# Kernel tuning notes

Hardware: AMD Instinct MI355X
Metric: run time of the kernel (lower is better)

The kernel has to match this reference:

```python
import jax, jax.numpy as jnp
import numpy as np

NULL_IDX = 0  # word_to_idx['<NULL>']
N, T, D, WV, H, V = 128, 65, 512, 128, 128, 10000


def setup_inputs() -> dict:
    key = jax.random.key(0)
    ks = jax.random.split(key, 12)
    scale = 0.02
    return {
        "features": jax.random.normal(ks[0], (N, D), dtype=jnp.float32),
        "captions": jax.random.randint(ks[1], (N, T), 0, V, dtype=jnp.int32),
        # TemporalAffine(input_dim, hidden_dim)
        "W_proj": jax.random.normal(ks[2], (D, H), dtype=jnp.float32) * scale,
        "b_proj": jnp.zeros((H,), dtype=jnp.float32),
        # nn.Embedding(vocab_size, wordvec_dim)
        "embed": jax.random.normal(ks[3], (V, WV), dtype=jnp.float32) * scale,
        # nn.RNN(wordvec_dim, hidden_dim, num_layers=1) weights
        "W_ih": jax.random.normal(ks[4], (H, WV), dtype=jnp.float32) * scale,
        "W_hh": jax.random.normal(ks[5], (H, H), dtype=jnp.float32) * scale,
        "b_ih": jnp.zeros((H,), dtype=jnp.float32),
        "b_hh": jnp.zeros((H,), dtype=jnp.float32),
        # TemporalAffine(hidden_dim, vocab_size)
        "W_vocab": jax.random.normal(ks[6], (H, V), dtype=jnp.float32) * scale,
        "b_vocab": jnp.zeros((V,), dtype=jnp.float32),
    }


def reference(features, captions, W_proj, b_proj, embed, W_ih, W_hh, b_ih, b_hh, W_vocab, b_vocab):
    captions_in = captions[:, :-1]   # (N, T-1)
    captions_out = captions[:, 1:]   # (N, T-1)
    mask = (captions_out != NULL_IDX).astype(jnp.float32)

    # initial hidden state: affine projection of image features (no tanh)
    h0 = features @ W_proj + b_proj                      # (N, H)

    # word embeddings, time-major for scan
    x = embed[captions_in]                               # (N, T-1, WV)
    x_tm = jnp.swapaxes(x, 0, 1)                          # (T-1, N, WV)

    def step(h_prev, x_t):
        # vanilla RNN cell: tanh(x W_ih^T + b_ih + h W_hh^T + b_hh)
        h_new = jnp.tanh(x_t @ W_ih.T + b_ih + h_prev @ W_hh.T + b_hh)
        return h_new, h_new

    _, hs = jax.lax.scan(step, h0, x_tm)                  # (T-1, N, H)
    h = jnp.swapaxes(hs, 0, 1)                            # (N, T-1, H)

    # temporal affine to vocab scores
    scores = h @ W_vocab + b_vocab                        # (N, T-1, V)

    # temporal softmax loss, masked, averaged over batch size N
    logp = jax.nn.log_softmax(scores, axis=-1)
    nll = -jnp.take_along_axis(logp, captions_out[..., None], axis=-1)[..., 0]
    loss = jnp.sum(nll * mask) / captions.shape[0]
    return loss
```

## Files before the change

kernel.cpp:

```cpp
#include <hip/hip_runtime.h>
#include <hip/hip_bf16.h>
#include <math.h>

typedef __attribute__((ext_vector_type(8))) short short8;
typedef __attribute__((ext_vector_type(4))) float f32x4;
typedef __attribute__((ext_vector_type(4))) unsigned int u32x4;

#define NB   128
#define TT   64
#define DD   512
#define HH   128
#define WVD  128
#define VV   10000
#define VP   10048
#define NROW (NB*TT)
#define NTILE (VP/64)
#define VT   32
#define TILE_BYTES 16384
#define LOG2E 1.44269504088896f
#define LN2   0.69314718055995f

__device__ __forceinline__ unsigned short f2bf(float x) {
  union { float f; unsigned int u; } v; v.f = x;
  unsigned int r = v.u + 0x7fffu + ((v.u >> 16) & 1u);
  return (unsigned short)(r >> 16);
}
__device__ __forceinline__ float bf2f(unsigned short u) {
  union { unsigned int i; float f; } v; v.i = ((unsigned int)u) << 16; return v.f;
}
__device__ __forceinline__ short8 cvt2bf8(f32x4 a, f32x4 b) {
  short8 t;
  t[0]=(short)f2bf(a[0]); t[1]=(short)f2bf(a[1]);
  t[2]=(short)f2bf(a[2]); t[3]=(short)f2bf(a[3]);
  t[4]=(short)f2bf(b[0]); t[5]=(short)f2bf(b[1]);
  t[6]=(short)f2bf(b[2]); t[7]=(short)f2bf(b[3]);
  return t;
}

__global__ __launch_bounds__(256) void k_main(
    const float* __restrict__ Wv, unsigned short* __restrict__ Wvt,
    const float* __restrict__ bv, float* __restrict__ expbv,
    float* __restrict__ out,
    const float* __restrict__ features, const float* __restrict__ Wp,
    const float* __restrict__ bp,
    const int* __restrict__ captions, const float* __restrict__ embed,
    const float* __restrict__ Wih, const float* __restrict__ bih,
    const float* __restrict__ bhh, const float* __restrict__ Whh,
    unsigned short* __restrict__ hsb) {
  __shared__ __align__(16) char smem[99328];
  int b = blockIdx.x, tid = threadIdx.x;

  if (b >= 128) {
    if (b < 442) {
      float (*tile)[65] = (float (*)[65])smem;
      int tb = b - 128;
      int bvv = (tb >> 1) * 64;
      int bk  = (tb & 1) * 64;
      int tv = tid & 63;
      int tk0 = tid >> 6;
      #pragma unroll
      for (int kk = 0; kk < 64; kk += 4) {
        int k = bk + kk + tk0;
        int v = bvv + tv;
        tile[kk + tk0][tv] = (v < VV) ? Wv[(size_t)k*VV + v] : 0.f;
      }
      __syncthreads();
      int tk = tid & 63;
      int tv0 = tid >> 6;
      #pragma unroll
      for (int vv = 0; vv < 64; vv += 4) {
        int v = bvv + vv + tv0;
        Wvt[(size_t)v*HH + bk + tk] = f2bf(tile[tk][vv + tv0]);
      }
    } else if (b < 482) {
      int v = (b - 442)*256 + tid;
      if (v < VP) expbv[v] = (v < VV) ? __expf(bv[v]) : 0.f;
    } else {
      if (tid == 0) out[0] = 0.f;
    }
    return;
  }

  int n = b;
  float* xl            = (float*)smem;
  unsigned short* hl   = (unsigned short*)(smem + 32768);
  char* xbf            = smem + 49152;
  char* wihbf          = smem + 65536;
  float* hbuf          = (float*)(smem + 98304);
  int w = tid >> 6, l = tid & 63;
  int l4 = l >> 4, lc = l & 15;

  {
    float* fl  = (float*)(smem + 32768);
    f32x4* red = (f32x4*)(smem + 32768 + 2048);
    fl[tid]       = features[n*DD + tid];
    fl[tid + 256] = features[n*DD + 256 + tid];
    __syncthreads();
    int jq = (tid & 31) * 4;
    int ks = tid >> 5;
    f32x4 acc = {0.f,0.f,0.f,0.f};
    const float* wp = Wp + (size_t)(ks*64)*HH + jq;
    #pragma unroll 4
    for (int k = 0; k < 64; ++k) {
      f32x4 wv = *(const f32x4*)(wp + (size_t)k*HH);
      acc += fl[ks*64 + k] * wv;
    }
    red[ks*32 + (tid & 31)] = acc;
    __syncthreads();
    if (tid < 32) {
      f32x4 s = red[tid];
      #pragma unroll
      for (int i = 1; i < 8; ++i) s += red[i*32 + tid];
      s += *(const f32x4*)(bp + tid*4);
      *(f32x4*)(hbuf + tid*4) = s;
    }
  }

  {
    int row = tid >> 1, half = tid & 1;
    const float* src = Wih + (size_t)row*WVD + half*64;
    #pragma unroll
    for (int i = 0; i < 8; ++i) {
      f32x4 a = *(const f32x4*)(src + i*8);
      f32x4 c = *(const f32x4*)(src + i*8 + 4);
      int chunk = half*8 + i;
      *(short8*)(wihbf + row*256 + ((chunk << 4) ^ ((row & 7) << 4))) = cvt2bf8(a, c);
    }
    int rt = tid >> 2, seg = tid & 3;
    int token = captions[n*65 + rt];
    const float* xs = embed + (size_t)token*WVD + seg*32;
    #pragma unroll
    for (int i = 0; i < 4; ++i) {
      f32x4 a = *(const f32x4*)(xs + i*8);
      f32x4 c = *(const f32x4*)(xs + i*8 + 4);
      int chunk = seg*4 + i;
      *(short8*)(xbf + rt*256 + ((chunk << 4) ^ ((rt & 7) << 4))) = cvt2bf8(a, c);
    }
  }
  int j = w*32 + (l & 31);
  int kb = (l >> 5) * 64;
  float wr_[64];
  const float* wsrc = Whh + (size_t)j*HH + kb;
  #pragma unroll
  for (int i = 0; i < 16; ++i) {
    f32x4 v = *(const f32x4*)(wsrc + i*4);
    wr_[i*4+0]=v[0]; wr_[i*4+1]=v[1]; wr_[i*4+2]=v[2]; wr_[i*4+3]=v[3];
  }
  __syncthreads();

  {
    short8 axf[4];
    int rowa = w*16 + lc;
    #pragma unroll
    for (int ks = 0; ks < 4; ++ks)
      axf[ks] = *(const short8*)(xbf + rowa*256 + (((ks*4 + l4) << 4) ^ ((rowa & 7) << 4)));
    #pragma unroll
    for (int ct = 0; ct < 8; ++ct) {
      int rowb = ct*16 + lc;
      f32x4 acc = {0.f,0.f,0.f,0.f};
      #pragma unroll
      for (int ks = 0; ks < 4; ++ks) {
        short8 bf = *(const short8*)(wihbf + rowb*256 + (((ks*4 + l4) << 4) ^ ((rowb & 7) << 4)));
        acc = __builtin_amdgcn_mfma_f32_16x16x32_bf16(axf[ks], bf, acc, 0, 0, 0);
      }
      int col = ct*16 + lc;
      float bb = bih[col] + bhh[col];
      #pragma unroll
      for (int jj = 0; jj < 4; ++jj)
        xl[(w*16 + l4*4 + jj)*HH + col] = acc[jj] + bb;
    }
  }
  __syncthreads();

  int cur = 0;
  for (int t = 0; t < TT; ++t) {
    float s0=0.f, s1=0.f, s2=0.f, s3=0.f;
    const float* hr = hbuf + cur*HH + kb;
    #pragma unroll
    for (int i = 0; i < 16; ++i) {
      f32x4 hv = *(const f32x4*)(hr + i*4);
      s0 += hv[0]*wr_[i*4+0]; s1 += hv[1]*wr_[i*4+1];
      s2 += hv[2]*wr_[i*4+2]; s3 += hv[3]*wr_[i*4+3];
    }
    float s = (s0+s1)+(s2+s3);
    s += __shfl_xor(s, 32);
    float v = s + xl[t*HH + j];
    float e = __builtin_amdgcn_exp2f(v * (2.0f*LOG2E));
    float h = 1.0f - 2.0f*__builtin_amdgcn_rcpf(e + 1.0f);
    if (l < 32) {
      hbuf[(cur^1)*HH + j] = h;
      hl[t*HH + j] = f2bf(h * LOG2E);
    }
    __syncthreads();
    cur ^= 1;
  }
  unsigned short* dst = hsb + (size_t)n*TT*HH;
  #pragma unroll
  for (int it = 0; it < 4; ++it) {
    int o = it*256 + tid;
    *(u32x4*)(dst + o*8) = *(const u32x4*)(hl + o*8);
  }
}

__global__ __launch_bounds__(256) void k_loss(
    const unsigned short* __restrict__ hsb,
    const unsigned short* __restrict__ wvt,
    const float* __restrict__ expbv,
    float* __restrict__ se_part) {
  __shared__ unsigned short bt[2][TILE_BYTES/2];
  int tid = threadIdx.x;
  int w = tid >> 6, l = tid & 63;
  int l4 = l >> 4, lc = l & 15;
  int rb = blockIdx.x >> 5;
  int vt = blockIdx.x & 31;
  int wrow = rb*256 + w*64;

  short8 af[4][4];
  #pragma unroll
  for (int sm = 0; sm < 4; ++sm)
    #pragma unroll
    for (int ks = 0; ks < 4; ++ks)
      af[sm][ks] = *(const short8*)(hsb + (size_t)(wrow + sm*16 + lc)*HH + ks*32 + l4*8);

  int T = (lc & 7) << 4;
  int sb[4];
  #pragma unroll
  for (int ks = 0; ks < 4; ++ks) sb[ks] = ((ks*64) + l4*16) ^ T;

#define STAGE(bufi, ct) do {                                                  \
    const char* _gb = (const char*)wvt + (size_t)(ct)*TILE_BYTES;             \
    _Pragma("unroll")                                                         \
    for (int q = 0; q < 4; ++q) {                                             \
      int _off = w*4096 + q*1024 + l*16;                                      \
      int _src = _off ^ (((_off >> 8) & 7) << 4);                             \
      __builtin_amdgcn_global_load_lds(                                       \
        (const __attribute__((address_space(1))) void*)(_gb + _src),          \
        (__attribute__((address_space(3))) void*)((char*)&bt[bufi][0] + w*4096 + q*1024), \
        16, 0, 0);                                                            \
    }                                                                         \
  } while (0)

#define EBLOAD(dst, ct) do {                                                  \
    const float* _e = expbv + (ct)*64 + lc;                                   \
    dst[0] = _e[0]; dst[1] = _e[16]; dst[2] = _e[32]; dst[3] = _e[48];        \
  } while (0)

#define COMPUTE(bufi, ebv_) do {                                              \
    const char* _Bb = (const char*)&bt[bufi][0];                              \
    _Pragma("unroll")                                                         \
    for (int st = 0; st < 4; ++st) {                                          \
      const char* _Bs = _Bb + st*4096 + lc*256;                               \
      short8 _b0 = *(const short8*)(_Bs + sb[0]);                             \
      short8 _b1 = *(const short8*)(_Bs + sb[1]);                             \
      short8 _b2 = *(const short8*)(_Bs + sb[2]);                             \
      short8 _b3 = *(const short8*)(_Bs + sb[3]);                             \
      float _eb = ebv_[st];                                                   \
      _Pragma("unroll")                                                       \
      for (int sm = 0; sm < 4; ++sm) {                                        \
        f32x4 _acc = {0.f,0.f,0.f,0.f};                                       \
        _acc = __builtin_amdgcn_mfma_f32_16x16x32_bf16(af[sm][0], _b0, _acc, 0,0,0); \
        _acc = __builtin_amdgcn_mfma_f32_16x16x32_bf16(af[sm][1], _b1, _acc, 0,0,0); \
        _acc = __builtin_amdgcn_mfma_f32_16x16x32_bf16(af[sm][2], _b2, _acc, 0,0,0); \
        _acc = __builtin_amdgcn_mfma_f32_16x16x32_bf16(af[sm][3], _b3, _acc, 0,0,0); \
        _Pragma("unroll")                                                     \
        for (int jj = 0; jj < 4; ++jj)                                        \
          se[sm][jj] = fmaf(__builtin_amdgcn_exp2f(_acc[jj]), _eb, se[sm][jj]); \
      }                                                                       \
    }                                                                         \
  } while (0)

  float se[4][4] = {{0.f}};
  float ebc[4], ebn[4];
  STAGE(0, vt);
  EBLOAD(ebc, vt);
  __syncthreads();
  int i = 0;
  for (;;) {
    int nextct = vt + (i+1)*VT;
    if (nextct < NTILE) { STAGE((i+1)&1, nextct); EBLOAD(ebn, nextct); }
    COMPUTE(i&1, ebc);
    if (nextct >= NTILE) break;
    __syncthreads();
    ebc[0]=ebn[0]; ebc[1]=ebn[1]; ebc[2]=ebn[2]; ebc[3]=ebn[3];
    ++i;
  }

  #pragma unroll
  for (int sm = 0; sm < 4; ++sm)
    #pragma unroll
    for (int jj = 0; jj < 4; ++jj) {
      float v = se[sm][jj];
      v += __shfl_xor(v, 1); v += __shfl_xor(v, 2);
      v += __shfl_xor(v, 4); v += __shfl_xor(v, 8);
      se[sm][jj] = v;
    }
  if (lc == 0) {
    #pragma unroll
    for (int sm = 0; sm < 4; ++sm)
      #pragma unroll
      for (int jj = 0; jj < 4; ++jj)
        se_part[(size_t)vt*NROW + wrow + sm*16 + l4*4 + jj] = se[sm][jj];
  }
#undef STAGE
#undef EBLOAD
#undef COMPUTE
}

__global__ __launch_bounds__(256) void k_final(
    const unsigned short* __restrict__ hsb,
    const unsigned short* __restrict__ wvt,
    const float* __restrict__ bv,
    const float* __restrict__ se_part,
    const int* __restrict__ captions,
    float* __restrict__ out) {
  int tid = threadIdx.x;
  int w = tid >> 6, l = tid & 63;
  int row = blockIdx.x*32 + w*8 + (l >> 3);
  int seg = l & 7;
  int n = row >> 6, t = row & 63;
  int tg = captions[n*65 + t + 1];
  float sep = 0.f;
  #pragma unroll
  for (int i = 0; i < 4; ++i)
    sep += se_part[(size_t)(seg*4 + i)*NROW + row];
  float part = 0.f;
  if (tg != 0) {
    const unsigned short* a = hsb + (size_t)row*HH + seg*16;
    const unsigned short* bq = wvt + (size_t)tg*HH + seg*16;
    short8 a0 = *(const short8*)a, a1 = *(const short8*)(a+8);
    short8 b0 = *(const short8*)bq, b1 = *(const short8*)(bq+8);
    #pragma unroll
    for (int i = 0; i < 8; ++i) {
      part += bf2f((unsigned short)a0[i]) * bf2f((unsigned short)b0[i]);
      part += bf2f((unsigned short)a1[i]) * bf2f((unsigned short)b1[i]);
    }
  }
  part += __shfl_xor(part, 1); sep += __shfl_xor(sep, 1);
  part += __shfl_xor(part, 2); sep += __shfl_xor(sep, 2);
  part += __shfl_xor(part, 4); sep += __shfl_xor(sep, 4);
  if (seg == 0 && tg != 0) {
    float score = part * LN2 + bv[tg];
    float nll = logf(sep) - score;
    atomicAdd(out, nll * (1.0f/128.0f));
  }
}

extern "C" void kernel_launch(void* const* d_in, const int* in_sizes, int n_in,
                              void* d_out, int out_size, void* d_ws, size_t ws_size,
                              hipStream_t stream) {
  const float* features = (const float*)d_in[0];
  const int*   captions = (const int*)d_in[1];
  const float* W_proj   = (const float*)d_in[2];
  const float* b_proj   = (const float*)d_in[3];
  const float* embed    = (const float*)d_in[4];
  const float* W_ih     = (const float*)d_in[5];
  const float* W_hh     = (const float*)d_in[6];
  const float* b_ih     = (const float*)d_in[7];
  const float* b_hh     = (const float*)d_in[8];
  const float* W_vocab  = (const float*)d_in[9];
  const float* b_vocab  = (const float*)d_in[10];
  float* out = (float*)d_out;
  char* ws = (char*)d_ws;

  float*          se_part = (float*)(ws + 0x010000);
  unsigned short* hsb     = (unsigned short*)(ws + 0x410000);
  unsigned short* wvt     = (unsigned short*)(ws + 0x620000);
  float*          expbv   = (float*)(ws + 0x8A0000);

  hipLaunchKernelGGL(k_main, dim3(483), dim3(256), 0, stream,
                     W_vocab, wvt, b_vocab, expbv, out,
                     features, W_proj, b_proj, captions, embed,
                     W_ih, b_ih, b_hh, W_hh, hsb);
  hipLaunchKernelGGL(k_loss, dim3(32*VT), dim3(256), 0, stream,
                     hsb, wvt, expbv, se_part);
  hipLaunchKernelGGL(k_final, dim3(NROW/32), dim3(256), 0, stream,
                     hsb, wvt, b_vocab, se_part, captions, out);
}
```

Before: 94.17 us.

## Batch 16 sequences per block and run RNN recurrence on bf16 MFMA

The recurrent kernel now handles 16 batch rows per block instead of one, so only 8 blocks run the recurrence. Each step's h·W_hh product is done with bf16 MFMA, using weights held in registers and the hidden state kept in swizzled LDS. The input projection for step t+1 is computed inside step t, and each step's hidden output is written directly to global memory. The LOG2E scaling moves from the hidden state into the vocab weight transpose. This is meant to shorten the serial recurrence by replacing scalar FMA dot products with matrix ops. In exchange, the recurrence uses fewer CUs, keeps the hidden state in bf16, and puts per-step global embedding loads inside the loop.

Measured after the change: 141.6 us. +50.4%, slower.

```diff
diff --git a/kernel.cpp b/kernel.cpp
--- a/kernel.cpp
+++ b/kernel.cpp
@@ -47,13 +47,13 @@
     const float* __restrict__ Wih, const float* __restrict__ bih,
     const float* __restrict__ bhh, const float* __restrict__ Whh,
     unsigned short* __restrict__ hsb) {
-  __shared__ __align__(16) char smem[99328];
+  __shared__ __align__(16) char smem[16640];
   int b = blockIdx.x, tid = threadIdx.x;
 
-  if (b >= 128) {
-    if (b < 442) {
+  if (b >= 8) {
+    if (b < 322) {
       float (*tile)[65] = (float (*)[65])smem;
-      int tb = b - 128;
+      int tb = b - 8;
       int bvv = (tb >> 1) * 64;
       int bk  = (tb & 1) * 64;
       int tv = tid & 63;
@@ -70,10 +70,10 @@
       #pragma unroll
       for (int vv = 0; vv < 64; vv += 4) {
         int v = bvv + vv + tv0;
-        Wvt[(size_t)v*HH + bk + tk] = f2bf(tile[tk][vv + tv0]);
-      }
-    } else if (b < 482) {
-      int v = (b - 442)*256 + tid;
+        Wvt[(size_t)v*HH + bk + tk] = f2bf(tile[tk][vv + tv0] * LOG2E);
+      }
+    } else if (b < 362) {
+      int v = (b - 322)*256 + tid;
       if (v < VP) expbv[v] = (v < VV) ? __expf(bv[v]) : 0.f;
     } else {
       if (tid == 0) out[0] = 0.f;
@@ -81,124 +81,118 @@
     return;
   }
 
-  int n = b;
-  float* xl            = (float*)smem;
-  unsigned short* hl   = (unsigned short*)(smem + 32768);
-  char* xbf            = smem + 49152;
-  char* wihbf          = smem + 65536;
-  float* hbuf          = (float*)(smem + 98304);
+  int n0 = b * 16;
   int w = tid >> 6, l = tid & 63;
   int l4 = l >> 4, lc = l & 15;
 
+  short8 bw[2][4];
+  short8 bwih[2][4];
+  float bihbhh[2];
+  int jcol[2];
+  #pragma unroll
+  for (int c = 0; c < 2; ++c) {
+    int jc = (2*w + c)*16 + lc;
+    jcol[c] = jc;
+    bihbhh[c] = bih[jc] + bhh[jc];
+    #pragma unroll
+    for (int ks = 0; ks < 4; ++ks) {
+      const float* p = Whh + (size_t)jc*HH + ks*32 + l4*8;
+      bw[c][ks] = cvt2bf8(*(const f32x4*)p, *(const f32x4*)(p+4));
+      const float* q = Wih + (size_t)jc*WVD + ks*32 + l4*8;
+      bwih[c][ks] = cvt2bf8(*(const f32x4*)q, *(const f32x4*)(q+4));
+    }
+  }
+
   {
-    float* fl  = (float*)(smem + 32768);
-    f32x4* red = (f32x4*)(smem + 32768 + 2048);
-    fl[tid]       = features[n*DD + tid];
-    fl[tid + 256] = features[n*DD + 256 + tid];
-    __syncthreads();
-    int jq = (tid & 31) * 4;
-    int ks = tid >> 5;
-    f32x4 acc = {0.f,0.f,0.f,0.f};
-    const float* wp = Wp + (size_t)(ks*64)*HH + jq;
-    #pragma unroll 4
-    for (int k = 0; k < 64; ++k) {
-      f32x4 wv = *(const f32x4*)(wp + (size_t)k*HH);
-      acc += fl[ks*64 + k] * wv;
-    }
-    red[ks*32 + (tid & 31)] = acc;
-    __syncthreads();
-    if (tid < 32) {
-      f32x4 s = red[tid];
-      #pragma unroll
-      for (int i = 1; i < 8; ++i) s += red[i*32 + tid];
-      s += *(const f32x4*)(bp + tid*4);
-      *(f32x4*)(hbuf + tid*4) = s;
-    }
-  }
-
+    f32x4 acc0[2] = {{0.f,0.f,0.f,0.f},{0.f,0.f,0.f,0.f}};
+    #pragma unroll
+    for (int ks = 0; ks < 16; ++ks) {
+      int k0 = ks*32 + l4*8;
+      const float* fp = features + (size_t)(n0 + lc)*DD + k0;
+      short8 aF = cvt2bf8(*(const f32x4*)fp, *(const f32x4*)(fp+4));
+      #pragma unroll
+      for (int c = 0; c < 2; ++c) {
+        short8 bF;
+        #pragma unroll
+        for (int i2 = 0; i2 < 8; ++i2)
+          bF[i2] = (short)f2bf(Wp[(size_t)(k0+i2)*HH + jcol[c]]);
+        acc0[c] = __builtin_amdgcn_mfma_f32_16x16x32_bf16(aF, bF, acc0[c], 0,0,0);
+      }
+    }
+    #pragma unroll
+    for (int c = 0; c < 2; ++c) {
+      float bpv = bp[jcol[c]];
+      #pragma unroll
+      for (int jj = 0; jj < 4; ++jj) {
+        int s = l4*4 + jj;
+        *(unsigned short*)(smem + s*256 + ((jcol[c]*2) ^ ((s&7)<<4))) =
+            f2bf(acc0[c][jj] + bpv);
+      }
+    }
+  }
+
+  f32x4 xcur[2] = {{0.f,0.f,0.f,0.f},{0.f,0.f,0.f,0.f}};
   {
-    int row = tid >> 1, half = tid & 1;
-    const float* src = Wih + (size_t)row*WVD + half*64;
-    #pragma unroll
-    for (int i = 0; i < 8; ++i) {
-      f32x4 a = *(const f32x4*)(src + i*8);
-      f32x4 c = *(const f32x4*)(src + i*8 + 4);
-      int chunk = half*8 + i;
-      *(short8*)(wihbf + row*256 + ((chunk << 4) ^ ((row & 7) << 4))) = cvt2bf8(a, c);
-    }
-    int rt = tid >> 2, seg = tid & 3;
-    int token = captions[n*65 + rt];
-    const float* xs = embed + (size_t)token*WVD + seg*32;
-    #pragma unroll
-    for (int i = 0; i < 4; ++i) {
-      f32x4 a = *(const f32x4*)(xs + i*8);
-      f32x4 c = *(const f32x4*)(xs + i*8 + 4);
-      int chunk = seg*4 + i;
-      *(short8*)(xbf + rt*256 + ((chunk << 4) ^ ((rt & 7) << 4))) = cvt2bf8(a, c);
-    }
-  }
-  int j = w*32 + (l & 31);
-  int kb = (l >> 5) * 64;
-  float wr_[64];
-  const float* wsrc = Whh + (size_t)j*HH + kb;
-  #pragma unroll
-  for (int i = 0; i < 16; ++i) {
-    f32x4 v = *(const f32x4*)(wsrc + i*4);
-    wr_[i*4+0]=v[0]; wr_[i*4+1]=v[1]; wr_[i*4+2]=v[2]; wr_[i*4+3]=v[3];
+    int tok = captions[(n0 + lc)*65 + 0];
+    #pragma unroll
+    for (int ks = 0; ks < 4; ++ks) {
+      const float* ep = embed + (size_t)tok*WVD + ks*32 + l4*8;
+      short8 aX = cvt2bf8(*(const f32x4*)ep, *(const f32x4*)(ep+4));
+      xcur[0] = __builtin_amdgcn_mfma_f32_16x16x32_bf16(aX, bwih[0][ks], xcur[0], 0,0,0);
+      xcur[1] = __builtin_amdgcn_mfma_f32_16x16x32_bf16(aX, bwih[1][ks], xcur[1], 0,0,0);
+    }
   }
   __syncthreads();
 
-  {
-    short8 axf[4];
-    int rowa = w*16 + lc;
-    #pragma unroll
-    for (int ks = 0; ks < 4; ++ks)
-      axf[ks] = *(const short8*)(xbf + rowa*256 + (((ks*4 + l4) << 4) ^ ((rowa & 7) << 4)));
-    #pragma unroll
-    for (int ct = 0; ct < 8; ++ct) {
-      int rowb = ct*16 + lc;
-      f32x4 acc = {0.f,0.f,0.f,0.f};
-      #pragma unroll
-      for (int ks = 0; ks < 4; ++ks) {
-        short8 bf = *(const short8*)(wihbf + rowb*256 + (((ks*4 + l4) << 4) ^ ((rowb & 7) << 4)));
-        acc = __builtin_amdgcn_mfma_f32_16x16x32_bf16(axf[ks], bf, acc, 0, 0, 0);
-      }
-      int col = ct*16 + lc;
-      float bb = bih[col] + bhh[col];
-      #pragma unroll
-      for (int jj = 0; jj < 4; ++jj)
-        xl[(w*16 + l4*4 + jj)*HH + col] = acc[jj] + bb;
-    }
-  }
-  __syncthreads();
+  int fs = tid >> 4;
+  int fo = (tid & 15) * 16;
+  int frd = fo ^ ((fs & 7) << 4);
 
   int cur = 0;
   for (int t = 0; t < TT; ++t) {
-    float s0=0.f, s1=0.f, s2=0.f, s3=0.f;
-    const float* hr = hbuf + cur*HH + kb;
-    #pragma unroll
-    for (int i = 0; i < 16; ++i) {
-      f32x4 hv = *(const f32x4*)(hr + i*4);
-      s0 += hv[0]*wr_[i*4+0]; s1 += hv[1]*wr_[i*4+1];
-      s2 += hv[2]*wr_[i*4+2]; s3 += hv[3]*wr_[i*4+3];
-    }
-    float s = (s0+s1)+(s2+s3);
-    s += __shfl_xor(s, 32);
-    float v = s + xl[t*HH + j];
-    float e = __builtin_amdgcn_exp2f(v * (2.0f*LOG2E));
-    float h = 1.0f - 2.0f*__builtin_amdgcn_rcpf(e + 1.0f);
-    if (l < 32) {
-      hbuf[(cur^1)*HH + j] = h;
-      hl[t*HH + j] = f2bf(h * LOG2E);
+    short8 ah[4];
+    #pragma unroll
+    for (int ks = 0; ks < 4; ++ks)
+      ah[ks] = *(const short8*)(smem + cur*4096 + lc*256 +
+                                ((ks*64 + l4*16) ^ ((lc&7)<<4)));
+    f32x4 xnext[2] = {{0.f,0.f,0.f,0.f},{0.f,0.f,0.f,0.f}};
+    if (t < TT-1) {
+      int tok2 = captions[(n0 + lc)*65 + t + 1];
+      short8 aX[4];
+      #pragma unroll
+      for (int ks = 0; ks < 4; ++ks) {
+        const float* ep = embed + (size_t)tok2*WVD + ks*32 + l4*8;
+        aX[ks] = cvt2bf8(*(const f32x4*)ep, *(const f32x4*)(ep+4));
+      }
+      #pragma unroll
+      for (int ks = 0; ks < 4; ++ks) {
+        xnext[0] = __builtin_amdgcn_mfma_f32_16x16x32_bf16(aX[ks], bwih[0][ks], xnext[0], 0,0,0);
+        xnext[1] = __builtin_amdgcn_mfma_f32_16x16x32_bf16(aX[ks], bwih[1][ks], xnext[1], 0,0,0);
+      }
+    }
+    f32x4 acc[2] = {{0.f,0.f,0.f,0.f},{0.f,0.f,0.f,0.f}};
+    #pragma unroll
+    for (int ks = 0; ks < 4; ++ks) {
+      acc[0] = __builtin_amdgcn_mfma_f32_16x16x32_bf16(ah[ks], bw[0][ks], acc[0], 0,0,0);
+      acc[1] = __builtin_amdgcn_mfma_f32_16x16x32_bf16(ah[ks], bw[1][ks], acc[1], 0,0,0);
+    }
+    #pragma unroll
+    for (int c = 0; c < 2; ++c) {
+      #pragma unroll
+      for (int jj = 0; jj < 4; ++jj) {
+        int s = l4*4 + jj;
+        float v = acc[c][jj] + xcur[c][jj] + bihbhh[c];
+        float e = __builtin_amdgcn_exp2f(v * (2.0f*LOG2E));
+        float h = 1.0f - 2.0f*__builtin_amdgcn_rcpf(e + 1.0f);
+        *(unsigned short*)(smem + (cur^1)*4096 + s*256 +
+                           ((jcol[c]*2) ^ ((s&7)<<4))) = f2bf(h);
+      }
     }
     __syncthreads();
+    u32x4 fr = *(const u32x4*)(smem + (cur^1)*4096 + fs*256 + frd);
+    *(u32x4*)(hsb + ((size_t)(n0 + fs)*TT + t)*HH + (fo >> 1)) = fr;
+    xcur[0] = xnext[0]; xcur[1] = xnext[1];
     cur ^= 1;
-  }
-  unsigned short* dst = hsb + (size_t)n*TT*HH;
-  #pragma unroll
-  for (int it = 0; it < 4; ++it) {
-    int o = it*256 + tid;
-    *(u32x4*)(dst + o*8) = *(const u32x4*)(hl + o*8);
   }
 }
 
@@ -367,7 +361,7 @@
   unsigned short* wvt     = (unsigned short*)(ws + 0x620000);
   float*          expbv   = (float*)(ws + 0x8A0000);
 
-  hipLaunchKernelGGL(k_main, dim3(483), dim3(256), 0, stream,
+  hipLaunchKernelGGL(k_main, dim3(363), dim3(256), 0, stream,
                      W_vocab, wvt, b_vocab, expbv, out,
                      features, W_proj, b_proj, captions, embed,
                      W_ih, b_ih, b_hh, W_hh, hsb);
```
